# Kernel optimization log

Measured on AMD Instinct MI355X. Metric: run time of the kernel, lower is better.

## Reference

```python
import jax, jax.numpy as jnp
import numpy as np

B, S, D, H, DH, R = 8, 2048, 1024, 16, 64, 32
ALPHA, BETA, GAMMA = 0.2, 0.1, 0.1


def setup_inputs() -> dict:
    key = jax.random.key(0)
    ks = jax.random.split(key, 5)
    x = jax.random.normal(ks[0], (B, S, D), jnp.float32)
    q = jax.random.normal(ks[1], (B, S, H, DH), jnp.float32)
    k = jax.random.normal(ks[2], (B, S, H, DH), jnp.float32)
    v_value = jax.random.normal(ks[3], (B, S, D), jnp.float32)
    # reentry_proj weight (orthogonal init approximated by scaled gaussian)
    W = jax.random.normal(ks[4], (D, D), jnp.float32) * np.float32(np.sqrt(0.5 / D))
    return {"x": x, "q": q, "k": k, "v_value": v_value, "W": W}


def _normalize(t):
    return t / (jnp.linalg.norm(t, axis=-1, keepdims=True) + 1e-6)


def reference(x, q, k, v_value, W):
    Bz, Sl, Dm = x.shape
    qf = q.reshape(Bz, Sl, Dm).transpose(1, 0, 2)        # (S, B, D)
    kf = k.reshape(Bz, Sl, Dm).transpose(1, 0, 2)        # (S, B, D)
    vf = v_value.transpose(1, 0, 2)                      # (S, B, D)
    U0 = jnp.zeros((Bz, R, Dm), x.dtype)
    V0 = jnp.zeros((Bz, R, Dm), x.dtype)

    def step(carry, inp):
        U, V = carry
        q_t, k_t, v_t = inp                              # each (B, D)
        U = (1.0 - ALPHA) * U + ALPHA * _normalize(q_t)[:, None, :]
        V = (1.0 - ALPHA) * V + ALPHA * _normalize(k_t)[:, None, :]
        # y_t = (U^T V) v_t, computed factorized: never materialize dim x dim
        s = jnp.einsum('brd,bd->br', V, v_t)             # (B, R)
        y = jnp.einsum('brd,br->bd', U, s)               # (B, D)
        n = jnp.maximum(jnp.linalg.norm(y, axis=-1, keepdims=True), 1e-6)
        y = y / (1.0 + BETA * (n - 1.0))                 # homeostasis
        fb = GAMMA * (y @ W.T)                           # reentry projection
        return (U, V), fb

    (_, _), fbs = jax.lax.scan(step, (U0, V0), (qf, kf, vf))
    return x + fbs.transpose(1, 0, 2)                    # (B, S, D)
```

## Files before the change

kernel.cpp:

```cpp
#include <hip/hip_runtime.h>
#include <hip/hip_bf16.h>
#include <cstdint>
#include <cstddef>

#define B_ 8
#define S_ 2048
#define D_ 1024
#define RFAC 32.0f
#define ALPHA 0.2f
#define BETA 0.1f
#define GAMMA 0.1f
#define KW 32
#define TB 64
#define PF_ 8

typedef float f32x4_t __attribute__((ext_vector_type(4)));
typedef short bf16x8_t __attribute__((ext_vector_type(8)));

__device__ __forceinline__ unsigned short f2bf(float f) {
    unsigned u = __float_as_uint(f);
    u = (u + 0x7fffu + ((u >> 16) & 1u)) >> 16;
    return (unsigned short)u;
}
__device__ __forceinline__ float bf2f(unsigned short h) {
    return __uint_as_float(((unsigned)h) << 16);
}

__global__ __launch_bounds__(256) void normalize_k(const float* __restrict__ q,
                                                   const float* __restrict__ k,
                                                   unsigned short* __restrict__ qh,
                                                   unsigned short* __restrict__ kh,
                                                   float* __restrict__ rnq,
                                                   float* __restrict__ rnk) {
    int row  = blockIdx.x * 4 + (threadIdx.x >> 6);
    int lane = threadIdx.x & 63;
    const float4* qr = (const float4*)(q + (size_t)row * D_);
    const float4* kr = (const float4*)(k + (size_t)row * D_);
    ushort4* qo = (ushort4*)(qh + (size_t)row * D_);
    ushort4* ko = (ushort4*)(kh + (size_t)row * D_);
    float sq = 0.f, sk = 0.f;
#pragma unroll
    for (int j = 0; j < 4; ++j) {
        float4 a = qr[lane + 64 * j];
        float4 b = kr[lane + 64 * j];
        sq += a.x * a.x + a.y * a.y + a.z * a.z + a.w * a.w;
        sk += b.x * b.x + b.y * b.y + b.z * b.z + b.w * b.w;
        ushort4 oq, ok;
        oq.x = f2bf(a.x); oq.y = f2bf(a.y); oq.z = f2bf(a.z); oq.w = f2bf(a.w);
        ok.x = f2bf(b.x); ok.y = f2bf(b.y); ok.z = f2bf(b.z); ok.w = f2bf(b.w);
        qo[lane + 64 * j] = oq;
        ko[lane + 64 * j] = ok;
    }
#pragma unroll
    for (int off = 32; off > 0; off >>= 1) {
        sq += __shfl_xor(sq, off, 64);
        sk += __shfl_xor(sk, off, 64);
    }
    if (lane == 0) {
        rnq[row] = ALPHA / (sqrtf(sq) + 1e-6f);
        rnk[row] = ALPHA / (sqrtf(sk) + 1e-6f);
    }
}

__global__ __launch_bounds__(256) void wconv_k(const float* __restrict__ W,
                                               unsigned short* __restrict__ Wb) {
    int i = blockIdx.x * 256 + threadIdx.x;
    float4 w = ((const float4*)W)[i];
    ushort4 o;
    o.x = f2bf(w.x); o.y = f2bf(w.y); o.z = f2bf(w.z); o.w = f2bf(w.w);
    ((ushort4*)Wb)[i] = o;
}

__global__ __launch_bounds__(256) void ema_coef_k(const unsigned short* __restrict__ qh,
                                                  const unsigned short* __restrict__ kh,
                                                  const float* __restrict__ rnq,
                                                  const float* __restrict__ rnk,
                                                  const float* __restrict__ vv,
                                                  unsigned short* __restrict__ Ub,
                                                  float* __restrict__ coef) {
    __shared__ float sm[TB * 8];
    const int chunks = S_ / TB;
    int b  = blockIdx.x / chunks;
    int t0 = (blockIdx.x % chunks) * TB;
    int ts = t0 - KW; if (ts < 0) ts = 0;
    int tid = threadIdx.x;
    int lane = tid & 63, wave = tid >> 6;
    size_t bbase = (size_t)b * S_ * D_ + tid * 4;
    const unsigned short* qp = qh + bbase;
    const unsigned short* kp = kh + bbase;
    const float* vp = vv + bbase;
    unsigned short* up = Ub + bbase;
    const float* rq = rnq + b * S_;
    const float* rk = rnk + b * S_;

    ushort4 pq[PF_], pk[PF_];
    float4 pv[PF_];
    float paq[PF_], pak[PF_];
#pragma unroll
    for (int j = 0; j < PF_; ++j) {
        size_t o = (size_t)(ts + j) * D_;
        pq[j] = *(const ushort4*)(qp + o);
        pk[j] = *(const ushort4*)(kp + o);
        paq[j] = rq[ts + j];
        pak[j] = rk[ts + j];
        if (ts + j >= t0) pv[j] = *(const float4*)(vp + o);
    }
    float u0 = 0.f, u1 = 0.f, u2 = 0.f, u3 = 0.f;
    float v0 = 0.f, v1 = 0.f, v2 = 0.f, v3 = 0.f;
    const float om = 1.f - ALPHA;
    const int NI = t0 + TB - ts;
    const int tend = t0 + TB;
    for (int g = 0; g < NI; g += PF_) {
#pragma unroll
        for (int j = 0; j < PF_; ++j) {
            int t = ts + g + j;
            float aq = paq[j], ak = pak[j];
            u0 = om * u0 + aq * bf2f(pq[j].x); u1 = om * u1 + aq * bf2f(pq[j].y);
            u2 = om * u2 + aq * bf2f(pq[j].z); u3 = om * u3 + aq * bf2f(pq[j].w);
            v0 = om * v0 + ak * bf2f(pk[j].x); v1 = om * v1 + ak * bf2f(pk[j].y);
            v2 = om * v2 + ak * bf2f(pk[j].z); v3 = om * v3 + ak * bf2f(pk[j].w);
            if (t >= t0) {
                float uu = u0 * u0 + u1 * u1 + u2 * u2 + u3 * u3;
                float sd = v0 * pv[j].x + v1 * pv[j].y + v2 * pv[j].z + v3 * pv[j].w;
#pragma unroll
                for (int off = 32; off > 0; off >>= 1) {
                    uu += __shfl_xor(uu, off, 64);
                    sd += __shfl_xor(sd, off, 64);
                }
                if (lane == 0) {
                    sm[(t - t0) * 8 + wave * 2 + 0] = uu;
                    sm[(t - t0) * 8 + wave * 2 + 1] = sd;
                }
                ushort4 us;
                us.x = f2bf(u0); us.y = f2bf(u1); us.z = f2bf(u2); us.w = f2bf(u3);
                *(ushort4*)(up + (size_t)t * D_) = us;
            }
            int tf = t + PF_;
            int tc = tf < tend ? tf : tend - 1;
            size_t o2 = (size_t)tc * D_;
            pq[j] = *(const ushort4*)(qp + o2);
            pk[j] = *(const ushort4*)(kp + o2);
            paq[j] = rq[tc];
            pak[j] = rk[tc];
            if (tf >= t0) pv[j] = *(const float4*)(vp + o2);
        }
    }
    __syncthreads();
    if (tid < TB) {
        float uu = sm[tid * 8 + 0] + sm[tid * 8 + 2] + sm[tid * 8 + 4] + sm[tid * 8 + 6];
        float sd = sm[tid * 8 + 1] + sm[tid * 8 + 3] + sm[tid * 8 + 5] + sm[tid * 8 + 7];
        float nrm = RFAC * fabsf(sd) * sqrtf(uu);
        float n = fmaxf(nrm, 1e-6f);
        coef[b * S_ + t0 + tid] = GAMMA * RFAC * sd / (1.f + BETA * (n - 1.f));
    }
}

#define BM 256
#define BN 256
#define BK 64
#define NT (D_ / BK)

__global__ __launch_bounds__(512, 2) void gemm_k(const unsigned short* __restrict__ A,
                                                 const unsigned short* __restrict__ Bw,
                                                 const float* __restrict__ coef,
                                                 const float* __restrict__ x,
                                                 float* __restrict__ out) {
    const int N = D_, K = D_;
    __shared__ unsigned short lds[2 * 2 * BM * BK];
    int bid = blockIdx.x;
    int swz = (bid & 7) * 32 + (bid >> 3);
    int tm = swz >> 2, tn = swz & 3;
    int m0 = tm * BM, n0 = tn * BN;
    int tid = threadIdx.x;
    int lane = tid & 63;
    int wid = tid >> 6;
    int wm = wid >> 2, wn = wid & 3;
    int lr = lane & 15, lg = lane >> 4;

    f32x4_t acc[8][4];
#pragma unroll
    for (int i = 0; i < 8; ++i)
#pragma unroll
        for (int j = 0; j < 4; ++j)
            acc[i][j] = (f32x4_t){0.f, 0.f, 0.f, 0.f};

#define STAGE_HALF(buf, kt, h)                                                        \
    {                                                                                 \
        int isB = (h) >> 1;                                                           \
        const unsigned short* Gp =                                                    \
            (isB ? Bw + (size_t)n0 * K : A + (size_t)m0 * K) + (size_t)(kt) * BK;     \
        unsigned short* Lp = lds + (buf) * 32768 + isB * 16384;                       \
        _Pragma("unroll")                                                             \
        for (int i = 0; i < 2; ++i) {                                                 \
            int c = i * 512 + tid;                \
            int row = ((h) & 1) * 128 + (c >> 3);                                     \
            int cl = c & 7;                                                           \
            int gc = cl ^ (row & 7);                   \
            __builtin_amdgcn_global_load_lds(                                         \
                (const __attribute__((address_space(1))) void*)(Gp + (size_t)row * K + gc * 8), \
                (__attribute__((address_space(3))) void*)((char*)Lp + (((((h)&1)*128 + (c>>3)) * 8 + cl) * 16)), \
                16, 0, 0);                                                            \
        }                                                                             \
    }

    STAGE_HALF(0, 0, 0); STAGE_HALF(0, 0, 1); STAGE_HALF(0, 0, 2); STAGE_HALF(0, 0, 3);
    __syncthreads();

    for (int t = 0; t < NT; ++t) {
        const unsigned short* La = lds + (t & 1) * 32768;
        const unsigned short* Lb = La + 16384;
        int nb = (t + 1) & 1;
        bool more = (t + 1 < NT);
        bf16x8_t bfrag[4][2];
#pragma unroll
        for (int p = 0; p < 4; ++p) {
            if (p == 0) {
#pragma unroll
                for (int ni = 0; ni < 4; ++ni)
#pragma unroll
                    for (int kk = 0; kk < 2; ++kk) {
                        int row = wn * 64 + ni * 16 + lr;
                        int ch = (kk * 4 + lg) ^ (row & 7);
                        bfrag[ni][kk] = *(const bf16x8_t*)(Lb + (row * 8 + ch) * 8);
                    }
            }
            bf16x8_t afrag[2][2];
#pragma unroll
            for (int qq = 0; qq < 2; ++qq)
#pragma unroll
                for (int kk = 0; kk < 2; ++kk) {
                    int row = wm * 128 + p * 32 + qq * 16 + lr;
                    int ch = (kk * 4 + lg) ^ (row & 7);
                    afrag[qq][kk] = *(const bf16x8_t*)(La + (row * 8 + ch) * 8);
                }
            if (more) STAGE_HALF(nb, t + 1, p);
            __builtin_amdgcn_s_barrier();
            asm volatile("s_waitcnt lgkmcnt(0)" ::: "memory");
            __builtin_amdgcn_sched_barrier(0);
            __builtin_amdgcn_s_setprio(1);
#pragma unroll
            for (int qq = 0; qq < 2; ++qq)
#pragma unroll
                for (int ni = 0; ni < 4; ++ni)
#pragma unroll
                    for (int kk = 0; kk < 2; ++kk)
                        acc[p * 2 + qq][ni] = __builtin_amdgcn_mfma_f32_16x16x32_bf16(
                            afrag[qq][kk], bfrag[ni][kk], acc[p * 2 + qq][ni], 0, 0, 0);
            __builtin_amdgcn_s_setprio(0);
            if (p < 3) __builtin_amdgcn_s_barrier();
        }
        __syncthreads();
    }
#undef STAGE_HALF

#pragma unroll
    for (int mi = 0; mi < 8; ++mi) {
#pragma unroll
        for (int i = 0; i < 4; ++i) {
            int m = m0 + wm * 128 + mi * 16 + lg * 4 + i;
            float cf = coef[m];
#pragma unroll
            for (int ni = 0; ni < 4; ++ni) {
                int n = n0 + wn * 64 + ni * 16 + lr;
                size_t idx = (size_t)m * N + n;
                out[idx] = x[idx] + cf * acc[mi][ni][i];
            }
        }
    }
}

extern "C" void kernel_launch(void* const* d_in, const int* in_sizes, int n_in,
                              void* d_out, int out_size, void* d_ws, size_t ws_size,
                              hipStream_t stream) {
    const float* x  = (const float*)d_in[0];
    const float* q  = (const float*)d_in[1];
    const float* k  = (const float*)d_in[2];
    const float* vv = (const float*)d_in[3];
    const float* W  = (const float*)d_in[4];
    float* out = (float*)d_out;

    const size_t M = (size_t)B_ * S_;
    char* ws = (char*)d_ws;
    unsigned short* Ub = (unsigned short*)ws;
    unsigned short* Wb = (unsigned short*)(ws + M * D_ * 2);
    float* coef = (float*)(ws + M * D_ * 2 + (size_t)D_ * D_ * 2);
    float* rnq  = coef + M;
    float* rnk  = rnq + M;
    size_t needed = M * D_ * 2 + (size_t)D_ * D_ * 2 + 3 * M * 4;
    if (ws_size < needed) return;

    unsigned short* qh = (unsigned short*)d_out;
    unsigned short* kh = qh + M * D_;

    normalize_k<<<dim3(M / 4), dim3(256), 0, stream>>>(q, k, qh, kh, rnq, rnk);
    wconv_k<<<dim3((D_ * D_) / 1024), dim3(256), 0, stream>>>(W, Wb);
    ema_coef_k<<<dim3(B_ * (S_ / TB)), dim3(256), 0, stream>>>(qh, kh, rnq, rnk, vv, Ub, coef);
    gemm_k<<<dim3((M / BM) * (D_ / BN)), dim3(512), 0, stream>>>(Ub, Wb, coef, x, out);
}
```

Baseline: 127.7 us.

## Use smaller single-buffered GEMM tiles and process two rows per wave in normalize

The GEMM moves from 256x256 double-buffered tiles with 512 threads, split-phase prefetch and priority hints to simpler 128x128 single-buffered tiles with 256 threads. This yields more blocks and lower per-block LDS and register use, so more blocks can share a CU. The cost is that loads and MFMA no longer overlap within a block, and each tile reuses data less. Separately, the normalize kernel now has each wave handle two rows, issuing all loads before any compute to raise memory-level parallelism.

```diff
diff --git a/kernel.cpp b/kernel.cpp
--- a/kernel.cpp
+++ b/kernel.cpp
@@ -26,39 +26,62 @@
     return __uint_as_float(((unsigned)h) << 16);
 }
 
-__global__ __launch_bounds__(256) void normalize_k(const float* __restrict__ q,
-                                                   const float* __restrict__ k,
-                                                   unsigned short* __restrict__ qh,
-                                                   unsigned short* __restrict__ kh,
-                                                   float* __restrict__ rnq,
-                                                   float* __restrict__ rnk) {
-    int row  = blockIdx.x * 4 + (threadIdx.x >> 6);
-    int lane = threadIdx.x & 63;
-    const float4* qr = (const float4*)(q + (size_t)row * D_);
-    const float4* kr = (const float4*)(k + (size_t)row * D_);
-    ushort4* qo = (ushort4*)(qh + (size_t)row * D_);
-    ushort4* ko = (ushort4*)(kh + (size_t)row * D_);
-    float sq = 0.f, sk = 0.f;
+__global__ __launch_bounds__(256, 4) void normalize_k(const float* __restrict__ q,
+                                                      const float* __restrict__ k,
+                                                      unsigned short* __restrict__ qh,
+                                                      unsigned short* __restrict__ kh,
+                                                      float* __restrict__ rnq,
+                                                      float* __restrict__ rnk) {
+    int wave = threadIdx.x >> 6, lane = threadIdx.x & 63;
+    int row0 = blockIdx.x * 8 + wave * 2;
+    const float4* q0 = (const float4*)(q + (size_t)row0 * D_);
+    const float4* k0 = (const float4*)(k + (size_t)row0 * D_);
+    const float4* q1 = (const float4*)(q + (size_t)(row0 + 1) * D_);
+    const float4* k1 = (const float4*)(k + (size_t)(row0 + 1) * D_);
+    float4 a0[4], b0[4], a1[4], b1[4];
 #pragma unroll
     for (int j = 0; j < 4; ++j) {
-        float4 a = qr[lane + 64 * j];
-        float4 b = kr[lane + 64 * j];
-        sq += a.x * a.x + a.y * a.y + a.z * a.z + a.w * a.w;
-        sk += b.x * b.x + b.y * b.y + b.z * b.z + b.w * b.w;
-        ushort4 oq, ok;
-        oq.x = f2bf(a.x); oq.y = f2bf(a.y); oq.z = f2bf(a.z); oq.w = f2bf(a.w);
-        ok.x = f2bf(b.x); ok.y = f2bf(b.y); ok.z = f2bf(b.z); ok.w = f2bf(b.w);
-        qo[lane + 64 * j] = oq;
-        ko[lane + 64 * j] = ok;
+        a0[j] = q0[lane + 64 * j];
+        b0[j] = k0[lane + 64 * j];
+        a1[j] = q1[lane + 64 * j];
+        b1[j] = k1[lane + 64 * j];
+    }
+    float sq0 = 0.f, sk0 = 0.f, sq1 = 0.f, sk1 = 0.f;
+#pragma unroll
+    for (int j = 0; j < 4; ++j) {
+        sq0 += a0[j].x * a0[j].x + a0[j].y * a0[j].y + a0[j].z * a0[j].z + a0[j].w * a0[j].w;
+        sk0 += b0[j].x * b0[j].x + b0[j].y * b0[j].y + b0[j].z * b0[j].z + b0[j].w * b0[j].w;
+        sq1 += a1[j].x * a1[j].x + a1[j].y * a1[j].y + a1[j].z * a1[j].z + a1[j].w * a1[j].w;
+        sk1 += b1[j].x * b1[j].x + b1[j].y * b1[j].y + b1[j].z * b1[j].z + b1[j].w * b1[j].w;
+    }
+    ushort4* qo0 = (ushort4*)(qh + (size_t)row0 * D_);
+    ushort4* ko0 = (ushort4*)(kh + (size_t)row0 * D_);
+    ushort4* qo1 = (ushort4*)(qh + (size_t)(row0 + 1) * D_);
+    ushort4* ko1 = (ushort4*)(kh + (size_t)(row0 + 1) * D_);
+#pragma unroll
+    for (int j = 0; j < 4; ++j) {
+        ushort4 t;
+        t.x = f2bf(a0[j].x); t.y = f2bf(a0[j].y); t.z = f2bf(a0[j].z); t.w = f2bf(a0[j].w);
+        qo0[lane + 64 * j] = t;
+        t.x = f2bf(b0[j].x); t.y = f2bf(b0[j].y); t.z = f2bf(b0[j].z); t.w = f2bf(b0[j].w);
+        ko0[lane + 64 * j] = t;
+        t.x = f2bf(a1[j].x); t.y = f2bf(a1[j].y); t.z = f2bf(a1[j].z); t.w = f2bf(a1[j].w);
+        qo1[lane + 64 * j] = t;
+        t.x = f2bf(b1[j].x); t.y = f2bf(b1[j].y); t.z = f2bf(b1[j].z); t.w = f2bf(b1[j].w);
+        ko1[lane + 64 * j] = t;
     }
 #pragma unroll
     for (int off = 32; off > 0; off >>= 1) {
-        sq += __shfl_xor(sq, off, 64);
-        sk += __shfl_xor(sk, off, 64);
+        sq0 += __shfl_xor(sq0, off, 64);
+        sk0 += __shfl_xor(sk0, off, 64);
+        sq1 += __shfl_xor(sq1, off, 64);
+        sk1 += __shfl_xor(sk1, off, 64);
     }
     if (lane == 0) {
-        rnq[row] = ALPHA / (sqrtf(sq) + 1e-6f);
-        rnk[row] = ALPHA / (sqrtf(sk) + 1e-6f);
+        rnq[row0] = ALPHA / (sqrtf(sq0) + 1e-6f);
+        rnk[row0] = ALPHA / (sqrtf(sk0) + 1e-6f);
+        rnq[row0 + 1] = ALPHA / (sqrtf(sq1) + 1e-6f);
+        rnk[row0 + 1] = ALPHA / (sqrtf(sk1) + 1e-6f);
     }
 }
 
@@ -155,113 +178,86 @@
     }
 }
 
-#define BM 256
-#define BN 256
+#define BM 128
+#define BN 128
 #define BK 64
 #define NT (D_ / BK)
 
-__global__ __launch_bounds__(512, 2) void gemm_k(const unsigned short* __restrict__ A,
-                                                 const unsigned short* __restrict__ Bw,
-                                                 const float* __restrict__ coef,
-                                                 const float* __restrict__ x,
-                                                 float* __restrict__ out) {
+__global__ __launch_bounds__(256) void gemm_k(const unsigned short* __restrict__ A,
+                                              const unsigned short* __restrict__ Bw,
+                                              const float* __restrict__ coef,
+                                              const float* __restrict__ x,
+                                              float* __restrict__ out) {
     const int N = D_, K = D_;
-    __shared__ unsigned short lds[2 * 2 * BM * BK];
+    __shared__ unsigned short As[BM * BK];
+    __shared__ unsigned short Bs[BN * BK];
     int bid = blockIdx.x;
-    int swz = (bid & 7) * 32 + (bid >> 3);
-    int tm = swz >> 2, tn = swz & 3;
+    int swz = (bid & 7) * 128 + (bid >> 3);
+    int tn = swz & 7, tm = swz >> 3;
     int m0 = tm * BM, n0 = tn * BN;
     int tid = threadIdx.x;
     int lane = tid & 63;
     int wid = tid >> 6;
-    int wm = wid >> 2, wn = wid & 3;
+    int wr = wid >> 1, wc = wid & 1;
     int lr = lane & 15, lg = lane >> 4;
 
-    f32x4_t acc[8][4];
-#pragma unroll
-    for (int i = 0; i < 8; ++i)
+    f32x4_t acc[4][4];
+#pragma unroll
+    for (int i = 0; i < 4; ++i)
 #pragma unroll
         for (int j = 0; j < 4; ++j)
             acc[i][j] = (f32x4_t){0.f, 0.f, 0.f, 0.f};
 
-#define STAGE_HALF(buf, kt, h)                                                        \
-    {                                                                                 \
-        int isB = (h) >> 1;                                                           \
-        const unsigned short* Gp =                                                    \
-            (isB ? Bw + (size_t)n0 * K : A + (size_t)m0 * K) + (size_t)(kt) * BK;     \
-        unsigned short* Lp = lds + (buf) * 32768 + isB * 16384;                       \
-        _Pragma("unroll")                                                             \
-        for (int i = 0; i < 2; ++i) {                                                 \
-            int c = i * 512 + tid;                \
-            int row = ((h) & 1) * 128 + (c >> 3);                                     \
-            int cl = c & 7;                                                           \
-            int gc = cl ^ (row & 7);                   \
-            __builtin_amdgcn_global_load_lds(                                         \
-                (const __attribute__((address_space(1))) void*)(Gp + (size_t)row * K + gc * 8), \
-                (__attribute__((address_space(3))) void*)((char*)Lp + (((((h)&1)*128 + (c>>3)) * 8 + cl) * 16)), \
-                16, 0, 0);                                                            \
-        }                                                                             \
-    }
-
-    STAGE_HALF(0, 0, 0); STAGE_HALF(0, 0, 1); STAGE_HALF(0, 0, 2); STAGE_HALF(0, 0, 3);
-    __syncthreads();
-
     for (int t = 0; t < NT; ++t) {
-        const unsigned short* La = lds + (t & 1) * 32768;
-        const unsigned short* Lb = La + 16384;
-        int nb = (t + 1) & 1;
-        bool more = (t + 1 < NT);
-        bf16x8_t bfrag[4][2];
-#pragma unroll
-        for (int p = 0; p < 4; ++p) {
-            if (p == 0) {
+        const unsigned short* Ab = A + (size_t)m0 * K + t * BK;
+        const unsigned short* Bb = Bw + (size_t)n0 * K + t * BK;
+#pragma unroll
+        for (int i = 0; i < 4; ++i) {
+            int c = i * 256 + tid;
+            int row = c >> 3, cl = c & 7;
+            int gc = cl ^ (row & 7);
+            __builtin_amdgcn_global_load_lds(
+                (const __attribute__((address_space(1))) void*)(Ab + (size_t)row * K + gc * 8),
+                (__attribute__((address_space(3))) void*)((char*)As + c * 16), 16, 0, 0);
+            __builtin_amdgcn_global_load_lds(
+                (const __attribute__((address_space(1))) void*)(Bb + (size_t)row * K + gc * 8),
+                (__attribute__((address_space(3))) void*)((char*)Bs + c * 16), 16, 0, 0);
+        }
+        __syncthreads();
+#pragma unroll
+        for (int kk = 0; kk < 2; ++kk) {
+            bf16x8_t af[4], bfr[4];
+#pragma unroll
+            for (int mi = 0; mi < 4; ++mi) {
+                int row = wr * 64 + mi * 16 + lr;
+                int ch = (kk * 4 + lg) ^ (row & 7);
+                af[mi] = *(const bf16x8_t*)(As + (row * 8 + ch) * 8);
+            }
+#pragma unroll
+            for (int ni = 0; ni < 4; ++ni) {
+                int row = wc * 64 + ni * 16 + lr;
+                int ch = (kk * 4 + lg) ^ (row & 7);
+                bfr[ni] = *(const bf16x8_t*)(Bs + (row * 8 + ch) * 8);
+            }
+#pragma unroll
+            for (int mi = 0; mi < 4; ++mi)
 #pragma unroll
                 for (int ni = 0; ni < 4; ++ni)
-#pragma unroll
-                    for (int kk = 0; kk < 2; ++kk) {
-                        int row = wn * 64 + ni * 16 + lr;
-                        int ch = (kk * 4 + lg) ^ (row & 7);
-                        bfrag[ni][kk] = *(const bf16x8_t*)(Lb + (row * 8 + ch) * 8);
-                    }
-            }
-            bf16x8_t afrag[2][2];
-#pragma unroll
-            for (int qq = 0; qq < 2; ++qq)
-#pragma unroll
-                for (int kk = 0; kk < 2; ++kk) {
-                    int row = wm * 128 + p * 32 + qq * 16 + lr;
-                    int ch = (kk * 4 + lg) ^ (row & 7);
-                    afrag[qq][kk] = *(const bf16x8_t*)(La + (row * 8 + ch) * 8);
-                }
-            if (more) STAGE_HALF(nb, t + 1, p);
-            __builtin_amdgcn_s_barrier();
-            asm volatile("s_waitcnt lgkmcnt(0)" ::: "memory");
-            __builtin_amdgcn_sched_barrier(0);
-            __builtin_amdgcn_s_setprio(1);
-#pragma unroll
-            for (int qq = 0; qq < 2; ++qq)
-#pragma unroll
-                for (int ni = 0; ni < 4; ++ni)
-#pragma unroll
-                    for (int kk = 0; kk < 2; ++kk)
-                        acc[p * 2 + qq][ni] = __builtin_amdgcn_mfma_f32_16x16x32_bf16(
-                            afrag[qq][kk], bfrag[ni][kk], acc[p * 2 + qq][ni], 0, 0, 0);
-            __builtin_amdgcn_s_setprio(0);
-            if (p < 3) __builtin_amdgcn_s_barrier();
+                    acc[mi][ni] = __builtin_amdgcn_mfma_f32_16x16x32_bf16(
+                        af[mi], bfr[ni], acc[mi][ni], 0, 0, 0);
         }
         __syncthreads();
     }
-#undef STAGE_HALF
-
-#pragma unroll
-    for (int mi = 0; mi < 8; ++mi) {
+
+#pragma unroll
+    for (int mi = 0; mi < 4; ++mi) {
 #pragma unroll
         for (int i = 0; i < 4; ++i) {
-            int m = m0 + wm * 128 + mi * 16 + lg * 4 + i;
+            int m = m0 + wr * 64 + mi * 16 + lg * 4 + i;
             float cf = coef[m];
 #pragma unroll
             for (int ni = 0; ni < 4; ++ni) {
-                int n = n0 + wn * 64 + ni * 16 + lr;
+                int n = n0 + wc * 64 + ni * 16 + lr;
                 size_t idx = (size_t)m * N + n;
                 out[idx] = x[idx] + cf * acc[mi][ni][i];
             }
@@ -292,8 +288,8 @@
     unsigned short* qh = (unsigned short*)d_out;
     unsigned short* kh = qh + M * D_;
 
-    normalize_k<<<dim3(M / 4), dim3(256), 0, stream>>>(q, k, qh, kh, rnq, rnk);
+    normalize_k<<<dim3(M / 8), dim3(256), 0, stream>>>(q, k, qh, kh, rnq, rnk);
     wconv_k<<<dim3((D_ * D_) / 1024), dim3(256), 0, stream>>>(W, Wb);
     ema_coef_k<<<dim3(B_ * (S_ / TB)), dim3(256), 0, stream>>>(qh, kh, rnq, rnk, vv, Ub, coef);
-    gemm_k<<<dim3((M / BM) * (D_ / BN)), dim3(512), 0, stream>>>(Ub, Wb, coef, x, out);
-}
+    gemm_k<<<dim3((M / BM) * (D_ / BN)), dim3(256), 0, stream>>>(Ub, Wb, coef, x, out);
+}
```

After: 141.4 us. 10.7% more time.

## Drop bf16 q/k staging copies and restructure GEMM prefetch to two-tile lookahead

Applied to the files above, without the earlier changes.

The normalize kernel no longer writes bf16 copies of q and k. The EMA kernel now reads the fp32 inputs directly, which removes a full write-and-reread pass over two large tensors at the cost of reading fp32 rather than bf16 (cast-on-read). The GEMM mainloop now issues whole-tile async loads two tiles ahead, gated by vmcnt waits, in place of interleaving half-tile staging with per-phase barriers. The aim is better overlap of global loads with MFMA work. It relies on precise vmcnt accounting and on the buffer being reused only after all waves have passed the final barrier.

```diff
diff --git a/kernel.cpp b/kernel.cpp
--- a/kernel.cpp
+++ b/kernel.cpp
@@ -26,18 +26,14 @@
     return __uint_as_float(((unsigned)h) << 16);
 }
 
-__global__ __launch_bounds__(256) void normalize_k(const float* __restrict__ q,
-                                                   const float* __restrict__ k,
-                                                   unsigned short* __restrict__ qh,
-                                                   unsigned short* __restrict__ kh,
-                                                   float* __restrict__ rnq,
-                                                   float* __restrict__ rnk) {
+__global__ __launch_bounds__(256) void norms_k(const float* __restrict__ q,
+                                               const float* __restrict__ k,
+                                               float* __restrict__ rnq,
+                                               float* __restrict__ rnk) {
     int row  = blockIdx.x * 4 + (threadIdx.x >> 6);
     int lane = threadIdx.x & 63;
     const float4* qr = (const float4*)(q + (size_t)row * D_);
     const float4* kr = (const float4*)(k + (size_t)row * D_);
-    ushort4* qo = (ushort4*)(qh + (size_t)row * D_);
-    ushort4* ko = (ushort4*)(kh + (size_t)row * D_);
     float sq = 0.f, sk = 0.f;
 #pragma unroll
     for (int j = 0; j < 4; ++j) {
@@ -45,11 +41,6 @@
         float4 b = kr[lane + 64 * j];
         sq += a.x * a.x + a.y * a.y + a.z * a.z + a.w * a.w;
         sk += b.x * b.x + b.y * b.y + b.z * b.z + b.w * b.w;
-        ushort4 oq, ok;
-        oq.x = f2bf(a.x); oq.y = f2bf(a.y); oq.z = f2bf(a.z); oq.w = f2bf(a.w);
-        ok.x = f2bf(b.x); ok.y = f2bf(b.y); ok.z = f2bf(b.z); ok.w = f2bf(b.w);
-        qo[lane + 64 * j] = oq;
-        ko[lane + 64 * j] = ok;
     }
 #pragma unroll
     for (int off = 32; off > 0; off >>= 1) {
@@ -71,8 +62,8 @@
     ((ushort4*)Wb)[i] = o;
 }
 
-__global__ __launch_bounds__(256) void ema_coef_k(const unsigned short* __restrict__ qh,
-                                                  const unsigned short* __restrict__ kh,
+__global__ __launch_bounds__(256) void ema_coef_k(const float* __restrict__ q,
+                                                  const float* __restrict__ kk,
                                                   const float* __restrict__ rnq,
                                                   const float* __restrict__ rnk,
                                                   const float* __restrict__ vv,
@@ -86,21 +77,20 @@
     int tid = threadIdx.x;
     int lane = tid & 63, wave = tid >> 6;
     size_t bbase = (size_t)b * S_ * D_ + tid * 4;
-    const unsigned short* qp = qh + bbase;
-    const unsigned short* kp = kh + bbase;
+    const float* qp = q + bbase;
+    const float* kp = kk + bbase;
     const float* vp = vv + bbase;
     unsigned short* up = Ub + bbase;
     const float* rq = rnq + b * S_;
     const float* rk = rnk + b * S_;
 
-    ushort4 pq[PF_], pk[PF_];
-    float4 pv[PF_];
+    float4 pq[PF_], pk[PF_], pv[PF_];
     float paq[PF_], pak[PF_];
 #pragma unroll
     for (int j = 0; j < PF_; ++j) {
         size_t o = (size_t)(ts + j) * D_;
-        pq[j] = *(const ushort4*)(qp + o);
-        pk[j] = *(const ushort4*)(kp + o);
+        pq[j] = *(const float4*)(qp + o);
+        pk[j] = *(const float4*)(kp + o);
         paq[j] = rq[ts + j];
         pak[j] = rk[ts + j];
         if (ts + j >= t0) pv[j] = *(const float4*)(vp + o);
@@ -115,10 +105,10 @@
         for (int j = 0; j < PF_; ++j) {
             int t = ts + g + j;
             float aq = paq[j], ak = pak[j];
-            u0 = om * u0 + aq * bf2f(pq[j].x); u1 = om * u1 + aq * bf2f(pq[j].y);
-            u2 = om * u2 + aq * bf2f(pq[j].z); u3 = om * u3 + aq * bf2f(pq[j].w);
-            v0 = om * v0 + ak * bf2f(pk[j].x); v1 = om * v1 + ak * bf2f(pk[j].y);
-            v2 = om * v2 + ak * bf2f(pk[j].z); v3 = om * v3 + ak * bf2f(pk[j].w);
+            u0 = om * u0 + aq * pq[j].x; u1 = om * u1 + aq * pq[j].y;
+            u2 = om * u2 + aq * pq[j].z; u3 = om * u3 + aq * pq[j].w;
+            v0 = om * v0 + ak * pk[j].x; v1 = om * v1 + ak * pk[j].y;
+            v2 = om * v2 + ak * pk[j].z; v3 = om * v3 + ak * pk[j].w;
             if (t >= t0) {
                 float uu = u0 * u0 + u1 * u1 + u2 * u2 + u3 * u3;
                 float sd = v0 * pv[j].x + v1 * pv[j].y + v2 * pv[j].z + v3 * pv[j].w;
@@ -138,8 +128,8 @@
             int tf = t + PF_;
             int tc = tf < tend ? tf : tend - 1;
             size_t o2 = (size_t)tc * D_;
-            pq[j] = *(const ushort4*)(qp + o2);
-            pk[j] = *(const ushort4*)(kp + o2);
+            pq[j] = *(const float4*)(qp + o2);
+            pk[j] = *(const float4*)(kp + o2);
             paq[j] = rq[tc];
             pak[j] = rk[tc];
             if (tf >= t0) pv[j] = *(const float4*)(vp + o2);
@@ -202,15 +192,19 @@
                 16, 0, 0);                                                            \
         }                                                                             \
     }
-
-    STAGE_HALF(0, 0, 0); STAGE_HALF(0, 0, 1); STAGE_HALF(0, 0, 2); STAGE_HALF(0, 0, 3);
-    __syncthreads();
+#define STAGE_TILE(buf, kt)                                                           \
+    STAGE_HALF(buf, kt, 0); STAGE_HALF(buf, kt, 1);                                   \
+    STAGE_HALF(buf, kt, 2); STAGE_HALF(buf, kt, 3);
+
+    STAGE_TILE(0, 0);
+    STAGE_TILE(1, 1);
 
     for (int t = 0; t < NT; ++t) {
+        if (t == NT - 1) asm volatile("s_waitcnt vmcnt(0)" ::: "memory");
+        else             asm volatile("s_waitcnt vmcnt(8)" ::: "memory");
+        __builtin_amdgcn_s_barrier();
         const unsigned short* La = lds + (t & 1) * 32768;
         const unsigned short* Lb = La + 16384;
-        int nb = (t + 1) & 1;
-        bool more = (t + 1 < NT);
         bf16x8_t bfrag[4][2];
 #pragma unroll
         for (int p = 0; p < 4; ++p) {
@@ -218,23 +212,21 @@
 #pragma unroll
                 for (int ni = 0; ni < 4; ++ni)
 #pragma unroll
-                    for (int kk = 0; kk < 2; ++kk) {
+                    for (int kkk = 0; kkk < 2; ++kkk) {
                         int row = wn * 64 + ni * 16 + lr;
-                        int ch = (kk * 4 + lg) ^ (row & 7);
-                        bfrag[ni][kk] = *(const bf16x8_t*)(Lb + (row * 8 + ch) * 8);
+                        int ch = (kkk * 4 + lg) ^ (row & 7);
+                        bfrag[ni][kkk] = *(const bf16x8_t*)(Lb + (row * 8 + ch) * 8);
                     }
             }
             bf16x8_t afrag[2][2];
 #pragma unroll
             for (int qq = 0; qq < 2; ++qq)
 #pragma unroll
-                for (int kk = 0; kk < 2; ++kk) {
+                for (int kkk = 0; kkk < 2; ++kkk) {
                     int row = wm * 128 + p * 32 + qq * 16 + lr;
-                    int ch = (kk * 4 + lg) ^ (row & 7);
-                    afrag[qq][kk] = *(const bf16x8_t*)(La + (row * 8 + ch) * 8);
+                    int ch = (kkk * 4 + lg) ^ (row & 7);
+                    afrag[qq][kkk] = *(const bf16x8_t*)(La + (row * 8 + ch) * 8);
                 }
-            if (more) STAGE_HALF(nb, t + 1, p);
-            __builtin_amdgcn_s_barrier();
             asm volatile("s_waitcnt lgkmcnt(0)" ::: "memory");
             __builtin_amdgcn_sched_barrier(0);
             __builtin_amdgcn_s_setprio(1);
@@ -243,14 +235,15 @@
 #pragma unroll
                 for (int ni = 0; ni < 4; ++ni)
 #pragma unroll
-                    for (int kk = 0; kk < 2; ++kk)
+                    for (int kkk = 0; kkk < 2; ++kkk)
                         acc[p * 2 + qq][ni] = __builtin_amdgcn_mfma_f32_16x16x32_bf16(
-                            afrag[qq][kk], bfrag[ni][kk], acc[p * 2 + qq][ni], 0, 0, 0);
+                            afrag[qq][kkk], bfrag[ni][kkk], acc[p * 2 + qq][ni], 0, 0, 0);
             __builtin_amdgcn_s_setprio(0);
-            if (p < 3) __builtin_amdgcn_s_barrier();
+            __builtin_amdgcn_s_barrier();
         }
-        __syncthreads();
-    }
+        if (t + 2 < NT) { STAGE_TILE((t & 1), t + 2); }
+    }
+#undef STAGE_TILE
 #undef STAGE_HALF
 
 #pragma unroll
@@ -289,11 +282,8 @@
     size_t needed = M * D_ * 2 + (size_t)D_ * D_ * 2 + 3 * M * 4;
     if (ws_size < needed) return;
 
-    unsigned short* qh = (unsigned short*)d_out;
-    unsigned short* kh = qh + M * D_;
-
-    normalize_k<<<dim3(M / 4), dim3(256), 0, stream>>>(q, k, qh, kh, rnq, rnk);
+    norms_k<<<dim3(M / 4), dim3(256), 0, stream>>>(q, k, rnq, rnk);
     wconv_k<<<dim3((D_ * D_) / 1024), dim3(256), 0, stream>>>(W, Wb);
-    ema_coef_k<<<dim3(B_ * (S_ / TB)), dim3(256), 0, stream>>>(qh, kh, rnq, rnk, vv, Ub, coef);
+    ema_coef_k<<<dim3(B_ * (S_ / TB)), dim3(256), 0, stream>>>(q, k, rnq, rnk, vv, Ub, coef);
     gemm_k<<<dim3((M / BM) * (D_ / BN)), dim3(512), 0, stream>>>(Ub, Wb, coef, x, out);
 }
```

Measured after the change: 129.4 us. No clear change (+1.3%).
